# Kernel optimization log

Hardware: AMD Instinct MI355X
Metric: run time of the kernel (lower is better)

The kernel has to match this reference:

```python
import jax, jax.numpy as jnp
import numpy as np

B, S, H, L, A, V, NL = 16, 256, 768, 12, 12, 30522, 9
DH = H // A
FF = 4 * H


def _ln(x, g, b):
    m = x.mean(-1, keepdims=True)
    v = jnp.var(x, axis=-1, keepdims=True)
    return (x - m) * jax.lax.rsqrt(v + 1e-12) * g + b


def setup_inputs() -> dict:
    key = jax.random.key(0)
    ks = jax.random.split(key, 16)
    n = lambda k, shape: jax.random.normal(k, shape, jnp.float32) * 0.02
    return {
        "input_word_ids": jax.random.randint(ks[0], (B, S), 0, V, jnp.int32),
        "input_mask": jnp.ones((B, S), jnp.int32),
        "input_type_ids": jnp.zeros((B, S), jnp.int32),
        "valid_mask": jax.random.randint(ks[1], (B, S), 0, 2, jnp.int32),
        "word_emb": n(ks[2], (V, H)),
        "pos_emb": n(ks[3], (S, H)),
        "type_emb": n(ks[4], (2, H)),
        "emb_ln_g": jnp.ones((H,), jnp.float32),
        "emb_ln_b": jnp.zeros((H,), jnp.float32),
        "Wq": n(ks[5], (L, H, H)), "bq": jnp.zeros((L, H), jnp.float32),
        "Wk": n(ks[6], (L, H, H)), "bk": jnp.zeros((L, H), jnp.float32),
        "Wv": n(ks[7], (L, H, H)), "bv": jnp.zeros((L, H), jnp.float32),
        "Wo": n(ks[8], (L, H, H)), "bo": jnp.zeros((L, H), jnp.float32),
        "attn_ln_g": jnp.ones((L, H), jnp.float32),
        "attn_ln_b": jnp.zeros((L, H), jnp.float32),
        "W1": n(ks[9], (L, H, FF)), "b1": jnp.zeros((L, FF), jnp.float32),
        "W2": n(ks[10], (L, FF, H)), "b2": jnp.zeros((L, H), jnp.float32),
        "ffn_ln_g": jnp.ones((L, H), jnp.float32),
        "ffn_ln_b": jnp.zeros((L, H), jnp.float32),
        "cls_W": n(ks[11], (H, NL)),
        "cls_b": jnp.zeros((NL,), jnp.float32),
    }


def reference(input_word_ids, input_mask, input_type_ids, valid_mask,
              word_emb, pos_emb, type_emb, emb_ln_g, emb_ln_b,
              Wq, bq, Wk, bk, Wv, bv, Wo, bo, attn_ln_g, attn_ln_b,
              W1, b1, W2, b2, ffn_ln_g, ffn_ln_b, cls_W, cls_b):
    # --- BERT embeddings ---
    x = word_emb[input_word_ids] + pos_emb[None, :, :] + type_emb[input_type_ids]
    x = _ln(x, emb_ln_g, emb_ln_b)
    amask = (1.0 - input_mask.astype(jnp.float32))[:, None, None, :] * -10000.0

    # --- 12 post-LN transformer layers via scan over stacked weights ---
    def block(x, p):
        wq, bq_, wk, bk_, wv, bv_, wo, bo_, ag, ab, w1, b1_, w2, b2_, fg, fb = p
        q = (x @ wq + bq_).reshape(B, S, A, DH)
        k = (x @ wk + bk_).reshape(B, S, A, DH)
        v = (x @ wv + bv_).reshape(B, S, A, DH)
        s = jnp.einsum('bqhd,bkhd->bhqk', q, k) * (1.0 / float(np.sqrt(DH))) + amask
        a = jax.nn.softmax(s, axis=-1)
        ctx = jnp.einsum('bhqk,bkhd->bqhd', a, v).reshape(B, S, H)
        x = _ln(x + ctx @ wo + bo_, ag, ab)
        h = jax.nn.gelu(x @ w1 + b1_)
        x = _ln(x + h @ w2 + b2_, fg, fb)
        return x, None

    x, _ = jax.lax.scan(block, x, (Wq, bq, Wk, bk, Wv, bv, Wo, bo,
                                   attn_ln_g, attn_ln_b, W1, b1, W2, b2,
                                   ffn_ln_g, ffn_ln_b))

    # --- valid-mask token compaction: valid tokens to front, zero pad ---
    # stable argsort moves valid_mask==1 positions to the front, in order
    order = jnp.argsort(1 - valid_mask, axis=1)  # stable by default
    gathered = jnp.take_along_axis(x, order[:, :, None], axis=1)
    counts = valid_mask.sum(axis=1)  # [B]
    keep = (jnp.arange(S)[None, :] < counts[:, None])[:, :, None]
    valid_out = jnp.where(keep, gathered, jnp.zeros((), x.dtype))

    # dropout is identity (training=False default); softmax classifier head
    return jax.nn.softmax(valid_out @ cls_W + cls_b, axis=-1)
```

## Files before the change

### kernel.cpp

```cpp
#include <hip/hip_runtime.h>

#define TOKENS 4096
#define BATCH  16
#define SEQ    256
#define Hdim   768
#define FFdim  3072
#define NHEAD  12
#define NLBL   9
#define NLAYER 12
#define QKVS   2304

typedef unsigned short u16;
typedef __attribute__((ext_vector_type(8))) short short8;
typedef __attribute__((ext_vector_type(4))) float floatx4;

__device__ __forceinline__ float bf2f(u16 u) {
    union { unsigned int i; float f; } c; c.i = ((unsigned int)u) << 16; return c.f;
}
__device__ __forceinline__ u16 f2bf(float f) {
    union { float f; unsigned int i; } c; c.f = f;
    unsigned int u = c.i;
    u = u + 0x7fffu + ((u >> 16) & 1u);
    return (u16)(u >> 16);
}

#define GLOAD16(gp, lp) __builtin_amdgcn_global_load_lds( \
    (__attribute__((address_space(1))) void*)(gp), \
    (__attribute__((address_space(3))) void*)(lp), 16, 0, 0)

__global__ __launch_bounds__(256) void k_conv_layer(
    const float* __restrict__ Wq, const float* __restrict__ Wk,
    const float* __restrict__ Wv, const float* __restrict__ Wo,
    const float* __restrict__ W1, const float* __restrict__ W2,
    u16* __restrict__ qkvT, u16* __restrict__ oT,
    u16* __restrict__ w1T, u16* __restrict__ w2T)
{
    int bid = blockIdx.x;
    const float* src; u16* dst; int K, N, t;
    if (bid < 576) {
        int m = bid / 144; t = bid - m * 144;
        src = (m == 0) ? Wq : (m == 1) ? Wk : (m == 2) ? Wv : Wo;
        dst = (m < 3) ? (qkvT + (size_t)m * 768 * 768) : oT;
        K = 768; N = 768;
    } else if (bid < 1152) {
        t = bid - 576; src = W1; dst = w1T; K = 768; N = 3072;
    } else {
        t = bid - 1152; src = W2; dst = w2T; K = 3072; N = 768;
    }
    int ntn = N >> 6;
    int tk = t / ntn, tn = t - tk * ntn;

    __shared__ float ld[64][65];
    int tid = threadIdx.x;
    int rr = tid >> 4;
    int cc = (tid & 15) * 4;
#pragma unroll
    for (int i = 0; i < 4; i++) {
        int k = tk * 64 + rr + i * 16;
        float4 v = *(const float4*)(src + (size_t)k * N + tn * 64 + cc);
        ld[rr + i * 16][cc + 0] = v.x;
        ld[rr + i * 16][cc + 1] = v.y;
        ld[rr + i * 16][cc + 2] = v.z;
        ld[rr + i * 16][cc + 3] = v.w;
    }
    __syncthreads();
    int n  = tid >> 2;
    int kc = (tid & 3) * 16;
    union { u16 h[16]; uint4 v[2]; } ob;
#pragma unroll
    for (int j = 0; j < 16; j++) ob.h[j] = f2bf(ld[kc + j][n]);
    u16* op = dst + (size_t)(tn * 64 + n) * K + tk * 64 + kc;
    *(uint4*)(op)     = ob.v[0];
    *(uint4*)(op + 8) = ob.v[1];
}

__global__ void k_biascat(const float* __restrict__ bq, const float* __restrict__ bk,
                          const float* __restrict__ bv, float* __restrict__ o)
{
    int l = blockIdx.x, t = threadIdx.x;
    o[l * QKVS + t]        = bq[l * Hdim + t];
    o[l * QKVS + 768 + t]  = bk[l * Hdim + t];
    o[l * QKVS + 1536 + t] = bv[l * Hdim + t];
}

template<int MODE, int BN>
__global__ __launch_bounds__(256) void k_gemm(const u16* __restrict__ Ag, const u16* __restrict__ Bg,
                                              const float* __restrict__ bias, void* __restrict__ outp,
                                              int N, int K)
{
    constexpr int NFR = BN / 32;
    __shared__ u16 As[2][128 * 32];
    __shared__ u16 Bs[2][BN * 32];
    const int tid  = threadIdx.x;
    const int lane = tid & 63, w = tid >> 6;
    const int wr = w >> 1, wc = w & 1;
    const int quad = lane >> 4, l16 = lane & 15;
    const int m0 = blockIdx.y * 128, n0 = blockIdx.x * BN;

    const int r0 = tid >> 2, c0 = (tid & 3) * 8;
    const u16* a0 = Ag + (size_t)(m0 + r0) * K + c0;
    const u16* a1 = a0 + (size_t)64 * K;
    const u16* b0 = Bg + (size_t)(n0 + r0) * K + c0;
    const u16* b1 = b0 + (size_t)64 * K;
    const int lofs0 = w * 512;
    const int lofs1 = 2048 + w * 512;

    const floatx4 vzero = {0.f, 0.f, 0.f, 0.f};
    floatx4 acc[4][NFR];
#pragma unroll
    for (int i = 0; i < 4; i++)
#pragma unroll
        for (int j = 0; j < NFR; j++) acc[i][j] = vzero;

    const int NT = K >> 5;

    GLOAD16(a0, &As[0][lofs0]);
    GLOAD16(a1, &As[0][lofs1]);
    GLOAD16(b0, &Bs[0][lofs0]);
    if constexpr (BN == 128) GLOAD16(b1, &Bs[0][lofs1]);

    for (int t = 0; t < NT; t++) {
        const int cur = t & 1, nxt = cur ^ 1;
        if (t + 1 < NT) {
            const int k1 = (t + 1) << 5;
            GLOAD16(a0 + k1, &As[nxt][lofs0]);
            GLOAD16(a1 + k1, &As[nxt][lofs1]);
            GLOAD16(b0 + k1, &Bs[nxt][lofs0]);
            if constexpr (BN == 128) {
                GLOAD16(b1 + k1, &Bs[nxt][lofs1]);
                asm volatile("s_waitcnt vmcnt(4)" ::: "memory");
            } else {
                asm volatile("s_waitcnt vmcnt(3)" ::: "memory");
            }
        } else {
            asm volatile("s_waitcnt vmcnt(0)" ::: "memory");
        }
        __builtin_amdgcn_sched_barrier(0);
        __builtin_amdgcn_s_barrier();
        __builtin_amdgcn_sched_barrier(0);

        short8 af[4], bfr[NFR];
#pragma unroll
        for (int mt = 0; mt < 4; mt++)
            af[mt]  = *(const short8*)(&As[cur][(wr * 64 + mt * 16 + l16) * 32 + quad * 8]);
#pragma unroll
        for (int nt = 0; nt < NFR; nt++)
            bfr[nt] = *(const short8*)(&Bs[cur][(wc * (BN / 2) + nt * 16 + l16) * 32 + quad * 8]);
#pragma unroll
        for (int mt = 0; mt < 4; mt++)
#pragma unroll
            for (int nt = 0; nt < NFR; nt++)
                acc[mt][nt] = __builtin_amdgcn_mfma_f32_16x16x32_bf16(af[mt], bfr[nt], acc[mt][nt], 0, 0, 0);

        __builtin_amdgcn_sched_barrier(0);
        __builtin_amdgcn_s_barrier();
        __builtin_amdgcn_sched_barrier(0);
    }

#pragma unroll
    for (int mt = 0; mt < 4; mt++) {
#pragma unroll
        for (int nt = 0; nt < NFR; nt++) {
            int col = n0 + wc * (BN / 2) + nt * 16 + l16;
            float bv = bias[col];
#pragma unroll
            for (int r = 0; r < 4; r++) {
                int row = m0 + wr * 64 + mt * 16 + quad * 4 + r;
                float vv = acc[mt][nt][r] + bv;
                if (MODE == 1) {
                    float t = 0.7978845608028654f * (vv + 0.044715f * vv * vv * vv);
                    vv = 0.5f * vv * (1.0f + tanhf(t));
                }
                if (MODE == 2) ((float*)outp)[(size_t)row * N + col] = vv;
                else          ((u16*)outp)[(size_t)row * N + col] = f2bf(vv);
            }
        }
    }
}

__global__ __launch_bounds__(256) void k_embed(const int* __restrict__ wid, const int* __restrict__ tidv,
                                               const float* __restrict__ we, const float* __restrict__ pe, const float* __restrict__ te,
                                               const float* __restrict__ g, const float* __restrict__ bb,
                                               float* __restrict__ xf, u16* __restrict__ xh)
{
    int i = blockIdx.x; int s = i & 255;
    int t = threadIdx.x;
    int wv = wid[i], tv = tidv[i];
    float e[3]; float sum = 0.f, sq = 0.f;
#pragma unroll
    for (int r = 0; r < 3; r++) {
        int j = t + r * 256;
        float x = we[(size_t)wv * Hdim + j] + pe[s * Hdim + j] + te[tv * Hdim + j];
        e[r] = x; sum += x; sq += x * x;
    }
    __shared__ float red[8];
    for (int off = 32; off; off >>= 1) { sum += __shfl_xor(sum, off); sq += __shfl_xor(sq, off); }
    if ((t & 63) == 0) { red[t >> 6] = sum; red[4 + (t >> 6)] = sq; }
    __syncthreads();
    sum = red[0] + red[1] + red[2] + red[3];
    sq  = red[4] + red[5] + red[6] + red[7];
    float mean = sum * (1.0f / Hdim);
    float var  = sq * (1.0f / Hdim) - mean * mean;
    float rstd = rsqrtf(var + 1e-12f);
#pragma unroll
    for (int r = 0; r < 3; r++) {
        int j = t + r * 256;
        float v = (e[r] - mean) * rstd * g[j] + bb[j];
        xf[(size_t)i * Hdim + j] = v;
        xh[(size_t)i * Hdim + j] = f2bf(v);
    }
}

__global__ __launch_bounds__(256) void k_addln(float* __restrict__ xf, const float* __restrict__ y,
                                               const float* __restrict__ g, const float* __restrict__ bb,
                                               u16* __restrict__ xh)
{
    int i = blockIdx.x; int t = threadIdx.x;
    float e[3]; float sum = 0.f, sq = 0.f;
#pragma unroll
    for (int r = 0; r < 3; r++) {
        int j = t + r * 256;
        float x = xf[(size_t)i * Hdim + j] + y[(size_t)i * Hdim + j];
        e[r] = x; sum += x; sq += x * x;
    }
    __shared__ float red[8];
    for (int off = 32; off; off >>= 1) { sum += __shfl_xor(sum, off); sq += __shfl_xor(sq, off); }
    if ((t & 63) == 0) { red[t >> 6] = sum; red[4 + (t >> 6)] = sq; }
    __syncthreads();
    sum = red[0] + red[1] + red[2] + red[3];
    sq  = red[4] + red[5] + red[6] + red[7];
    float mean = sum * (1.0f / Hdim);
    float var  = sq * (1.0f / Hdim) - mean * mean;
    float rstd = rsqrtf(var + 1e-12f);
#pragma unroll
    for (int r = 0; r < 3; r++) {
        int j = t + r * 256;
        float v = (e[r] - mean) * rstd * g[j] + bb[j];
        xf[(size_t)i * Hdim + j] = v;
        xh[(size_t)i * Hdim + j] = f2bf(v);
    }
}

__global__ __launch_bounds__(256, 2) void k_attn(const u16* __restrict__ qkv, const int* __restrict__ maskg,
                                                 u16* __restrict__ ctx)
{
    __shared__ u16 Vt[64 * 264];
    __shared__ u16 Ps[4 * 64 * 40];
    __shared__ float madd[256];
    int bh = blockIdx.x; int b = bh / NHEAD; int h = bh - b * NHEAD;
    int tid = threadIdx.x; int lane = tid & 63; int w = tid >> 6;
    int quad = lane >> 4, l16 = lane & 15;
    size_t baseq = (size_t)b * SEQ * QKVS + h * 64;
    size_t basec = (size_t)b * SEQ * Hdim + h * 64;

#pragma unroll
    for (int i = 0; i < 8; i++) {
        int c = tid + i * 256; int key = c >> 3; int cc = (c & 7) << 3;
        uint4 vv = *(const uint4*)(qkv + baseq + 1536 + (size_t)key * QKVS + cc);
        const u16* p16 = (const u16*)&vv;
#pragma unroll
        for (int e = 0; e < 8; e++) Vt[(cc + e) * 264 + key] = p16[e];
    }
    madd[tid] = (1.0f - (float)maskg[b * SEQ + tid]) * -10000.0f;
    __syncthreads();

    short8 aq[4][2];
#pragma unroll
    for (int mt = 0; mt < 4; mt++)
#pragma unroll
        for (int kf = 0; kf < 2; kf++)
            aq[mt][kf] = *(const short8*)(qkv + baseq + (size_t)(w * 64 + mt * 16 + l16) * QKVS + kf * 32 + quad * 8);

    const floatx4 vzero = {0.f, 0.f, 0.f, 0.f};
    floatx4 acc[4][4];
    float l_run[4][4];
#pragma unroll
    for (int a = 0; a < 4; a++)
#pragma unroll
        for (int r = 0; r < 4; r++) { acc[a][r] = vzero; l_run[a][r] = 0.f; }

    u16* Pw = &Ps[w * 64 * 40];

    for (int kc = 0; kc < 8; kc++) {
        floatx4 sc[4][2];
#pragma unroll
        for (int mt = 0; mt < 4; mt++) { sc[mt][0] = vzero; sc[mt][1] = vzero; }
#pragma unroll
        for (int kf = 0; kf < 2; kf++) {
            short8 bk_[2];
#pragma unroll
            for (int nt = 0; nt < 2; nt++)
                bk_[nt] = *(const short8*)(qkv + baseq + 768 + (size_t)(kc * 32 + nt * 16 + l16) * QKVS + kf * 32 + quad * 8);
#pragma unroll
            for (int mt = 0; mt < 4; mt++)
#pragma unroll
                for (int nt = 0; nt < 2; nt++)
                    sc[mt][nt] = __builtin_amdgcn_mfma_f32_16x16x32_bf16(aq[mt][kf], bk_[nt], sc[mt][nt], 0, 0, 0);
        }
        float madd0 = madd[kc * 32 + l16];
        float madd1 = madd[kc * 32 + 16 + l16];
#pragma unroll
        for (int mt = 0; mt < 4; mt++) {
#pragma unroll
            for (int r = 0; r < 4; r++) {
                float p0 = __expf(sc[mt][0][r] * 0.125f + madd0);
                float p1 = __expf(sc[mt][1][r] * 0.125f + madd1);
                float ls = p0 + p1;
#pragma unroll
                for (int off = 1; off < 16; off <<= 1) ls += __shfl_xor(ls, off);
                l_run[mt][r] += ls;
                int row = mt * 16 + quad * 4 + r;
                Pw[row * 40 + l16]      = f2bf(p0);
                Pw[row * 40 + 16 + l16] = f2bf(p1);
            }
        }
        short8 ap[4], bv_[4];
#pragma unroll
        for (int nt = 0; nt < 4; nt++)
            bv_[nt] = *(const short8*)(&Vt[(nt * 16 + l16) * 264 + kc * 32 + quad * 8]);
#pragma unroll
        for (int mt = 0; mt < 4; mt++)
            ap[mt] = *(const short8*)(&Pw[(mt * 16 + l16) * 40 + quad * 8]);
#pragma unroll
        for (int mt = 0; mt < 4; mt++)
#pragma unroll
            for (int nt = 0; nt < 4; nt++)
                acc[mt][nt] = __builtin_amdgcn_mfma_f32_16x16x32_bf16(ap[mt], bv_[nt], acc[mt][nt], 0, 0, 0);
    }
#pragma unroll
    for (int mt = 0; mt < 4; mt++)
#pragma unroll
        for (int r = 0; r < 4; r++) {
            float inv = 1.0f / l_run[mt][r];
            int sq_ = w * 64 + mt * 16 + quad * 4 + r;
#pragma unroll
            for (int nt = 0; nt < 4; nt++)
                ctx[basec + (size_t)sq_ * Hdim + nt * 16 + l16] = f2bf(acc[mt][nt][r] * inv);
        }
}

__global__ void k_compact(const int* __restrict__ vm, int* __restrict__ counts, int* __restrict__ srcidx)
{
    int b = blockIdx.x;
    if (threadIdx.x == 0) {
        int c = 0;
        for (int s = 0; s < SEQ; s++)
            if (vm[b * SEQ + s]) { srcidx[b * SEQ + c] = s; c++; }
        counts[b] = c;
    }
}

__global__ __launch_bounds__(256) void k_cls(const u16* __restrict__ x, const int* __restrict__ counts,
                                             const int* __restrict__ srcidx, const float* __restrict__ Wc,
                                             const float* __restrict__ bc, float* __restrict__ out)
{
    int w = threadIdx.x >> 6, lane = threadIdx.x & 63;
    int row = blockIdx.x * 4 + w;
    int b = row >> 8, s = row & 255;
    float acc[NLBL];
#pragma unroll
    for (int n = 0; n < NLBL; n++) acc[n] = 0.f;
    int cnt = counts[b];
    if (s < cnt) {
        int src = srcidx[b * SEQ + s];
        const u16* xr = x + (size_t)(b * SEQ + src) * Hdim;
        for (int j = lane; j < Hdim; j += 64) {
            float xv = bf2f(xr[j]);
#pragma unroll
            for (int n = 0; n < NLBL; n++) acc[n] += xv * Wc[j * NLBL + n];
        }
    }
#pragma unroll
    for (int n = 0; n < NLBL; n++)
        for (int off = 32; off; off >>= 1) acc[n] += __shfl_xor(acc[n], off);
    if (lane == 0) {
        float lg[NLBL]; float mx = -1e30f;
#pragma unroll
        for (int n = 0; n < NLBL; n++) { lg[n] = acc[n] + bc[n]; mx = fmaxf(mx, lg[n]); }
        float se = 0.f;
#pragma unroll
        for (int n = 0; n < NLBL; n++) { lg[n] = __expf(lg[n] - mx); se += lg[n]; }
        float inv = 1.0f / se;
#pragma unroll
        for (int n = 0; n < NLBL; n++) out[(size_t)row * NLBL + n] = lg[n] * inv;
    }
}

extern "C" void kernel_launch(void* const* d_in, const int* in_sizes, int n_in,
                              void* d_out, int out_size, void* d_ws, size_t ws_size,
                              hipStream_t stream)
{
    (void)in_sizes; (void)n_in; (void)out_size; (void)ws_size;
    const int* word_ids = (const int*)d_in[0];
    const int* in_mask  = (const int*)d_in[1];
    const int* type_ids = (const int*)d_in[2];
    const int* valid    = (const int*)d_in[3];
    const float* word_emb = (const float*)d_in[4];
    const float* pos_emb  = (const float*)d_in[5];
    const float* type_emb = (const float*)d_in[6];
    const float* eg = (const float*)d_in[7];
    const float* eb = (const float*)d_in[8];
    const float* Wq = (const float*)d_in[9];  const float* bq = (const float*)d_in[10];
    const float* Wk = (const float*)d_in[11]; const float* bk = (const float*)d_in[12];
    const float* Wv = (const float*)d_in[13]; const float* bv = (const float*)d_in[14];
    const float* Wo = (const float*)d_in[15]; const float* bo = (const float*)d_in[16];
    const float* ag = (const float*)d_in[17]; const float* ab = (const float*)d_in[18];
    const float* W1 = (const float*)d_in[19]; const float* b1 = (const float*)d_in[20];
    const float* W2 = (const float*)d_in[21]; const float* b2 = (const float*)d_in[22];
    const float* fg = (const float*)d_in[23]; const float* fb = (const float*)d_in[24];
    const float* Wc = (const float*)d_in[25]; const float* bc = (const float*)d_in[26];
    float* out = (float*)d_out;

    char* p = (char*)d_ws;
    int* counts = (int*)p;
    int* srcidx = (int*)(p + 1024);
    p += 65536;
    float* x_f32 = (float*)p; p += (size_t)TOKENS * Hdim * 4;
    u16* x_h  = (u16*)p; p += (size_t)TOKENS * Hdim * 2;
    float* tmpf = (float*)p; p += (size_t)TOKENS * Hdim * 4;
    u16* qkv_h = (u16*)p; p += (size_t)TOKENS * QKVS * 2;
    u16* c_h  = (u16*)p; p += (size_t)TOKENS * Hdim * 2;
    u16* h_h  = qkv_h;
    u16* wqkvT = (u16*)p; p += (size_t)QKVS * Hdim * 2;
    u16* woT   = (u16*)p; p += (size_t)Hdim * Hdim * 2;
    u16* w1T   = (u16*)p; p += (size_t)FFdim * Hdim * 2;
    u16* w2T   = (u16*)p; p += (size_t)Hdim * FFdim * 2;
    float* bqkv = (float*)p; p += (size_t)NLAYER * QKVS * 4;

    k_embed<<<TOKENS, 256, 0, stream>>>(word_ids, type_ids, word_emb, pos_emb, type_emb, eg, eb, x_f32, x_h);
    k_compact<<<BATCH, 64, 0, stream>>>(valid, counts, srcidx);
    k_biascat<<<NLAYER, 768, 0, stream>>>(bq, bk, bv, bqkv);

    for (int l = 0; l < NLAYER; l++) {
        size_t HH = (size_t)Hdim * Hdim;
        size_t HF = (size_t)Hdim * FFdim;
        k_conv_layer<<<1728, 256, 0, stream>>>(Wq + l * HH, Wk + l * HH, Wv + l * HH, Wo + l * HH,
                                               W1 + l * HF, W2 + l * HF, wqkvT, woT, w1T, w2T);
        k_gemm<0, 128><<<dim3(18, 32), 256, 0, stream>>>(x_h, wqkvT, bqkv + l * QKVS, qkv_h, QKVS, Hdim);
        k_attn<<<BATCH * NHEAD, 256, 0, stream>>>(qkv_h, in_mask, c_h);
        k_gemm<2, 64><<<dim3(12, 32), 256, 0, stream>>>(c_h, woT, bo + l * Hdim, tmpf, Hdim, Hdim);
        k_addln<<<TOKENS, 256, 0, stream>>>(x_f32, tmpf, ag + l * Hdim, ab + l * Hdim, x_h);
        k_gemm<1, 128><<<dim3(24, 32), 256, 0, stream>>>(x_h, w1T, b1 + l * FFdim, h_h, FFdim, Hdim);
        k_gemm<2, 64><<<dim3(12, 32), 256, 0, stream>>>(h_h, w2T, b2 + l * Hdim, tmpf, Hdim, FFdim);
        k_addln<<<TOKENS, 256, 0, stream>>>(x_f32, tmpf, fg + l * Hdim, fb + l * Hdim, x_h);
    }
    k_cls<<<TOKENS / 4, 256, 0, stream>>>(x_h, counts, srcidx, Wc, bc, out);
}
```

Baseline: 2.597 ms.

## Convert all layer weights in one launch and triple-buffer GEMM tile loads

All twelve layers' weight transposes and bf16 conversions now run in a single up-front kernel into per-layer workspace slices, replacing twelve per-layer conversion launches inside the layer loop. The GEMM mainloop moves from double to triple buffering in LDS, issuing loads two K-steps ahead with adjusted vmcnt waits. This aims to hide global-load latency and remove launch and serialization overhead. In exchange it uses more workspace memory and more LDS per block, which may lower occupancy.

After: 2.644 ms. No clear change (+1.8%).

```diff
diff --git a/kernel.cpp b/kernel.cpp
--- a/kernel.cpp
+++ b/kernel.cpp
@@ -28,24 +28,28 @@
     (__attribute__((address_space(1))) void*)(gp), \
     (__attribute__((address_space(3))) void*)(lp), 16, 0, 0)
 
-__global__ __launch_bounds__(256) void k_conv_layer(
+__global__ __launch_bounds__(256) void k_conv_all(
     const float* __restrict__ Wq, const float* __restrict__ Wk,
     const float* __restrict__ Wv, const float* __restrict__ Wo,
     const float* __restrict__ W1, const float* __restrict__ W2,
     u16* __restrict__ qkvT, u16* __restrict__ oT,
     u16* __restrict__ w1T, u16* __restrict__ w2T)
 {
+    const size_t HH = (size_t)768 * 768, HF = (size_t)768 * 3072;
     int bid = blockIdx.x;
+    int l = bid / 1728;
+    int r = bid - l * 1728;
     const float* src; u16* dst; int K, N, t;
-    if (bid < 576) {
-        int m = bid / 144; t = bid - m * 144;
-        src = (m == 0) ? Wq : (m == 1) ? Wk : (m == 2) ? Wv : Wo;
-        dst = (m < 3) ? (qkvT + (size_t)m * 768 * 768) : oT;
+    if (r < 576) {
+        int m = r / 144; t = r - m * 144;
+        src = ((m == 0) ? Wq : (m == 1) ? Wk : (m == 2) ? Wv : Wo) + l * HH;
+        dst = (m < 3) ? (qkvT + (size_t)l * QKVS * 768 + (size_t)m * 768 * 768)
+                      : (oT + l * HH);
         K = 768; N = 768;
-    } else if (bid < 1152) {
-        t = bid - 576; src = W1; dst = w1T; K = 768; N = 3072;
+    } else if (r < 1152) {
+        t = r - 576; src = W1 + l * HF; dst = w1T + l * HF; K = 768; N = 3072;
     } else {
-        t = bid - 1152; src = W2; dst = w2T; K = 3072; N = 768;
+        t = r - 1152; src = W2 + l * HF; dst = w2T + l * HF; K = 3072; N = 768;
     }
     int ntn = N >> 6;
     int tk = t / ntn, tn = t - tk * ntn;
@@ -89,8 +93,8 @@
                                               int N, int K)
 {
     constexpr int NFR = BN / 32;
-    __shared__ u16 As[2][128 * 32];
-    __shared__ u16 Bs[2][BN * 32];
+    __shared__ u16 As[3][128 * 32];
+    __shared__ u16 Bs[3][BN * 32];
     const int tid  = threadIdx.x;
     const int lane = tid & 63, w = tid >> 6;
     const int wr = w >> 1, wc = w & 1;
@@ -105,6 +109,13 @@
     const int lofs0 = w * 512;
     const int lofs1 = 2048 + w * 512;
 
+#define STAGE(kk, sl) do { \
+        GLOAD16(a0 + (kk), &As[sl][lofs0]); \
+        GLOAD16(a1 + (kk), &As[sl][lofs1]); \
+        GLOAD16(b0 + (kk), &Bs[sl][lofs0]); \
+        if constexpr (BN == 128) GLOAD16(b1 + (kk), &Bs[sl][lofs1]); \
+    } while (0)
+
     const floatx4 vzero = {0.f, 0.f, 0.f, 0.f};
     floatx4 acc[4][NFR];
 #pragma unroll
@@ -114,24 +125,19 @@
 
     const int NT = K >> 5;
 
-    GLOAD16(a0, &As[0][lofs0]);
-    GLOAD16(a1, &As[0][lofs1]);
-    GLOAD16(b0, &Bs[0][lofs0]);
-    if constexpr (BN == 128) GLOAD16(b1, &Bs[0][lofs1]);
-
-    for (int t = 0; t < NT; t++) {
-        const int cur = t & 1, nxt = cur ^ 1;
-        if (t + 1 < NT) {
-            const int k1 = (t + 1) << 5;
-            GLOAD16(a0 + k1, &As[nxt][lofs0]);
-            GLOAD16(a1 + k1, &As[nxt][lofs1]);
-            GLOAD16(b0 + k1, &Bs[nxt][lofs0]);
-            if constexpr (BN == 128) {
-                GLOAD16(b1 + k1, &Bs[nxt][lofs1]);
-                asm volatile("s_waitcnt vmcnt(4)" ::: "memory");
-            } else {
-                asm volatile("s_waitcnt vmcnt(3)" ::: "memory");
-            }
+    STAGE(0, 0);
+    STAGE(32, 1);
+
+    int cur = 0;
+    for (int t = 0; t < NT; ++t) {
+        int sl = cur + 2; if (sl >= 3) sl -= 3;
+        if (t + 2 < NT) {
+            STAGE((t + 2) << 5, sl);
+            if constexpr (BN == 128) asm volatile("s_waitcnt vmcnt(8)" ::: "memory");
+            else                     asm volatile("s_waitcnt vmcnt(6)" ::: "memory");
+        } else if (t + 1 < NT) {
+            if constexpr (BN == 128) asm volatile("s_waitcnt vmcnt(4)" ::: "memory");
+            else                     asm volatile("s_waitcnt vmcnt(3)" ::: "memory");
         } else {
             asm volatile("s_waitcnt vmcnt(0)" ::: "memory");
         }
@@ -139,13 +145,15 @@
         __builtin_amdgcn_s_barrier();
         __builtin_amdgcn_sched_barrier(0);
 
+        const u16* Ab = As[cur];
+        const u16* Bb = Bs[cur];
         short8 af[4], bfr[NFR];
 #pragma unroll
         for (int mt = 0; mt < 4; mt++)
-            af[mt]  = *(const short8*)(&As[cur][(wr * 64 + mt * 16 + l16) * 32 + quad * 8]);
+            af[mt]  = *(const short8*)(Ab + (wr * 64 + mt * 16 + l16) * 32 + quad * 8);
 #pragma unroll
         for (int nt = 0; nt < NFR; nt++)
-            bfr[nt] = *(const short8*)(&Bs[cur][(wc * (BN / 2) + nt * 16 + l16) * 32 + quad * 8]);
+            bfr[nt] = *(const short8*)(Bb + (wc * (BN / 2) + nt * 16 + l16) * 32 + quad * 8);
 #pragma unroll
         for (int mt = 0; mt < 4; mt++)
 #pragma unroll
@@ -155,7 +163,10 @@
         __builtin_amdgcn_sched_barrier(0);
         __builtin_amdgcn_s_barrier();
         __builtin_amdgcn_sched_barrier(0);
-    }
+
+        cur = (cur == 2) ? 0 : cur + 1;
+    }
+#undef STAGE
 
 #pragma unroll
     for (int mt = 0; mt < 4; mt++) {
@@ -421,27 +432,27 @@
     u16* qkv_h = (u16*)p; p += (size_t)TOKENS * QKVS * 2;
     u16* c_h  = (u16*)p; p += (size_t)TOKENS * Hdim * 2;
     u16* h_h  = qkv_h;
-    u16* wqkvT = (u16*)p; p += (size_t)QKVS * Hdim * 2;
-    u16* woT   = (u16*)p; p += (size_t)Hdim * Hdim * 2;
-    u16* w1T   = (u16*)p; p += (size_t)FFdim * Hdim * 2;
-    u16* w2T   = (u16*)p; p += (size_t)Hdim * FFdim * 2;
+    u16* wqkvT = (u16*)p; p += (size_t)NLAYER * QKVS * Hdim * 2;
+    u16* woT   = (u16*)p; p += (size_t)NLAYER * Hdim * Hdim * 2;
+    u16* w1T   = (u16*)p; p += (size_t)NLAYER * FFdim * Hdim * 2;
+    u16* w2T   = (u16*)p; p += (size_t)NLAYER * Hdim * FFdim * 2;
     float* bqkv = (float*)p; p += (size_t)NLAYER * QKVS * 4;
 
     k_embed<<<TOKENS, 256, 0, stream>>>(word_ids, type_ids, word_emb, pos_emb, type_emb, eg, eb, x_f32, x_h);
     k_compact<<<BATCH, 64, 0, stream>>>(valid, counts, srcidx);
     k_biascat<<<NLAYER, 768, 0, stream>>>(bq, bk, bv, bqkv);
+    k_conv_all<<<NLAYER * 1728, 256, 0, stream>>>(Wq, Wk, Wv, Wo, W1, W2, wqkvT, woT, w1T, w2T);
 
     for (int l = 0; l < NLAYER; l++) {
         size_t HH = (size_t)Hdim * Hdim;
         size_t HF = (size_t)Hdim * FFdim;
-        k_conv_layer<<<1728, 256, 0, stream>>>(Wq + l * HH, Wk + l * HH, Wv + l * HH, Wo + l * HH,
-                                               W1 + l * HF, W2 + l * HF, wqkvT, woT, w1T, w2T);
-        k_gemm<0, 128><<<dim3(18, 32), 256, 0, stream>>>(x_h, wqkvT, bqkv + l * QKVS, qkv_h, QKVS, Hdim);
+        k_gemm<0, 128><<<dim3(18, 32), 256, 0, stream>>>(x_h, wqkvT + (size_t)l * QKVS * Hdim,
+                                                         bqkv + l * QKVS, qkv_h, QKVS, Hdim);
         k_attn<<<BATCH * NHEAD, 256, 0, stream>>>(qkv_h, in_mask, c_h);
-        k_gemm<2, 64><<<dim3(12, 32), 256, 0, stream>>>(c_h, woT, bo + l * Hdim, tmpf, Hdim, Hdim);
+        k_gemm<2, 64><<<dim3(12, 32), 256, 0, stream>>>(c_h, woT + l * HH, bo + l * Hdim, tmpf, Hdim, Hdim);
         k_addln<<<TOKENS, 256, 0, stream>>>(x_f32, tmpf, ag + l * Hdim, ab + l * Hdim, x_h);
-        k_gemm<1, 128><<<dim3(24, 32), 256, 0, stream>>>(x_h, w1T, b1 + l * FFdim, h_h, FFdim, Hdim);
-        k_gemm<2, 64><<<dim3(12, 32), 256, 0, stream>>>(h_h, w2T, b2 + l * Hdim, tmpf, Hdim, FFdim);
+        k_gemm<1, 128><<<dim3(24, 32), 256, 0, stream>>>(x_h, w1T + l * HF, b1 + l * FFdim, h_h, FFdim, Hdim);
+        k_gemm<2, 64><<<dim3(12, 32), 256, 0, stream>>>(h_h, w2T + l * HF, b2 + l * Hdim, tmpf, Hdim, FFdim);
         k_addln<<<TOKENS, 256, 0, stream>>>(x_f32, tmpf, fg + l * Hdim, fb + l * Hdim, x_h);
     }
     k_cls<<<TOKENS / 4, 256, 0, stream>>>(x_h, counts, srcidx, Wc, bc, out);
```
